# Kernel tuning notes

Hardware: AMD Instinct MI355X
Metric: run time of the kernel (lower is better)

Reference implementation:

```python
import jax, jax.numpy as jnp
import numpy as np
from jax import lax

B, C = 16, 80
LEVELS = [(100, 128), (50, 64), (25, 32), (13, 16), (7, 8)]
STRIDES = [8, 16, 32, 64, 128]
SCORE_THR = 0.05
IOU_THR = 0.6
MAX_DET = 1000


def make_coords(h, w, stride):
    # FCOS: center of each cell in original-image coordinates, order (x, y)
    ys = jnp.arange(h, dtype=jnp.float32) * stride + stride // 2
    xs = jnp.arange(w, dtype=jnp.float32) * stride + stride // 2
    yy, xx = jnp.meshgrid(ys, xs, indexing='ij')
    return jnp.stack([xx.reshape(-1), yy.reshape(-1)], axis=-1)  # [h*w, 2]


def flatten_levels(feats):
    # list of [B, c, h, w] -> [B, sum(h*w), c]
    return jnp.concatenate(
        [f.transpose(0, 2, 3, 1).reshape(f.shape[0], -1, f.shape[1]) for f in feats], axis=1)


def pairwise_iou(boxes):
    # boxes [N,4]; +1 area convention, matching the torch box_nms
    x1, y1, x2, y2 = boxes[:, 0], boxes[:, 1], boxes[:, 2], boxes[:, 3]
    areas = (x2 - x1 + 1.0) * (y2 - y1 + 1.0)
    xmin = jnp.maximum(x1[:, None], x1[None, :])
    ymin = jnp.maximum(y1[:, None], y1[None, :])
    xmax = jnp.minimum(x2[:, None], x2[None, :])
    ymax = jnp.minimum(y2[:, None], y2[None, :])
    inter = jnp.clip(xmax - xmin, 0.0) * jnp.clip(ymax - ymin, 0.0)
    return inter / (areas[:, None] + areas[None, :] - inter)


def nms_keep_mask(boxes, valid, thr):
    # boxes are sorted by descending score (top_k sorted=True) -> greedy order = index order
    n = boxes.shape[0]
    iou = pairwise_iou(boxes)
    idx = jnp.arange(n)

    def body(i, sup):
        kept = jnp.logical_not(sup[i])
        return sup | (kept & (iou[i] > thr) & (idx > i))

    sup = lax.fori_loop(0, n, body, jnp.logical_not(valid))
    return valid & jnp.logical_not(sup)


def detect_forward(cls_feats, ctr_feats, reg_feats):
    cls_logits = flatten_levels(cls_feats)   # [B, P, C]
    ctr_logits = flatten_levels(ctr_feats)   # [B, P, 1]
    reg_preds = flatten_levels(reg_feats)    # [B, P, 4] (l, t, r, b)
    coords = jnp.concatenate(
        [make_coords(h, w, s) for (h, w), s in zip(LEVELS, STRIDES)], axis=0)  # [P, 2]

    cls_preds = jax.nn.sigmoid(cls_logits)
    ctr_preds = jax.nn.sigmoid(ctr_logits)[..., 0]
    cls_scores = jnp.max(cls_preds, axis=-1) * ctr_preds        # add_centerness=True
    cls_classes = jnp.argmax(cls_preds, axis=-1) + 1            # [B, P] int

    boxes = jnp.concatenate(
        [coords[None] - reg_preds[..., :2], coords[None] + reg_preds[..., 2:]], axis=-1)

    max_num = min(MAX_DET, cls_scores.shape[-1])
    scores_topk, topk_ind = lax.top_k(cls_scores, max_num)      # sorted descending
    classes_topk = jnp.take_along_axis(cls_classes, topk_ind, axis=1)
    boxes_topk = jnp.take_along_axis(boxes, topk_ind[..., None], axis=1)

    valid = scores_topk >= SCORE_THR
    # batched_nms class-offset trick
    max_coord = jnp.max(boxes_topk, axis=(1, 2), keepdims=True)
    offs = classes_topk.astype(boxes_topk.dtype)[..., None] * (max_coord + 1.0)
    boxes_for_nms = boxes_topk + offs

    keep = jax.vmap(lambda b, v: nms_keep_mask(b, v, IOU_THR))(boxes_for_nms, valid)
    keep_f = keep.astype(scores_topk.dtype)
    # fixed-shape masked outputs (torch version returns ragged per-batch lists)
    return scores_topk * keep_f, classes_topk * keep, boxes_topk * keep_f[..., None]


def setup_inputs() -> dict:
    key = jax.random.key(0)
    ks = jax.random.split(key, 3 * len(LEVELS))
    inp = {}
    for i, (h, w) in enumerate(LEVELS):
        inp[f'cls{i}'] = jax.random.normal(ks[3 * i], (B, C, h, w), jnp.float32)
        inp[f'ctr{i}'] = jax.random.normal(ks[3 * i + 1], (B, 1, h, w), jnp.float32)
        # positive ltrb offsets of plausible magnitude
        inp[f'reg{i}'] = jax.random.uniform(ks[3 * i + 2], (B, 4, h, w), jnp.float32) * 64.0 + 1.0
    return inp


def reference(cls0, cls1, cls2, cls3, cls4, ctr0, ctr1, ctr2, ctr3, ctr4,
              reg0, reg1, reg2, reg3, reg4):
    return detect_forward([cls0, cls1, cls2, cls3, cls4],
                          [ctr0, ctr1, ctr2, ctr3, ctr4],
                          [reg0, reg1, reg2, reg3, reg4])
```

## Files before the change

### kernel.cpp

```cpp
#include <hip/hip_runtime.h>
#include <stdint.h>

#define NANCH 17064
#define BATCH 16
#define NCLS 80
#define KDET 1000
#define SCORE_THR 0.05f
#define IOU_THR 0.6f

typedef unsigned long long u64;
typedef unsigned int u32;

__device__ __forceinline__ float sigf(float x) { return 1.0f / (1.0f + expf(-x)); }

__device__ __forceinline__ void decode_anchor(int n, int& l, int& h, int& w) {
  if (n < 12800)      { l = 0; h = n >> 7;               w = n & 127; }
  else if (n < 16000) { l = 1; int r = n - 12800; h = r >> 6; w = r & 63; }
  else if (n < 16800) { l = 2; int r = n - 16000; h = r >> 5; w = r & 31; }
  else if (n < 17008) { l = 3; int r = n - 16800; h = r >> 4; w = r & 15; }
  else                { l = 4; int r = n - 17008; h = r >> 3; w = r & 7; }
}

__device__ __forceinline__ u32 fenc(float f) {
  u32 u = __float_as_uint(f);
  return (u & 0x80000000u) ? ~u : (u | 0x80000000u);
}
__device__ __forceinline__ float fdec(u32 e) {
  u32 u = (e & 0x80000000u) ? (e ^ 0x80000000u) : ~e;
  return __uint_as_float(u);
}

__global__ __launch_bounds__(256, 4) void k_score(
    const float* __restrict__ cls0, const float* __restrict__ ctr0,
    const float* __restrict__ cls1, const float* __restrict__ ctr1,
    const float* __restrict__ cls2, const float* __restrict__ ctr2,
    const float* __restrict__ cls3, const float* __restrict__ ctr3,
    const float* __restrict__ cls4, const float* __restrict__ ctr4,
    u32* __restrict__ sb, u32* __restrict__ cl8)
{
  __shared__ float sm[4][64][5];
  __shared__ u32 sa[4][64];

  const int x = threadIdx.x;
  const int y = threadIdx.y;
  const int b = blockIdx.y;
  int q = blockIdx.x * 64 + x;
  const bool act = (q < NANCH / 4);
  int qc = act ? q : (NANCH / 4 - 1);
  int n = qc * 4;

  const float* cp; const float* tp; int hw, off;
  if (n < 12800)      { cp = cls0; tp = ctr0; hw = 12800; off = n; }
  else if (n < 16000) { cp = cls1; tp = ctr1; hw = 3200;  off = n - 12800; }
  else if (n < 16800) { cp = cls2; tp = ctr2; hw = 800;   off = n - 16000; }
  else if (n < 17008) { cp = cls3; tp = ctr3; hw = 208;   off = n - 16800; }
  else                { cp = cls4; tp = ctr4; hw = 56;    off = n - 17008; }
  const float4* base = (const float4*)(cp + (size_t)b * NCLS * hw + off);
  const int s4 = hw >> 2;
  const int cb = y * 20;

  float4 v[20];
#pragma unroll
  for (int cc = 0; cc < 20; ++cc) v[cc] = base[(size_t)(cb + cc) * s4];

  float m0 = -1.0f, m1 = -1.0f, m2 = -1.0f, m3 = -1.0f;
  int a0 = 0, a1 = 0, a2 = 0, a3 = 0;
#pragma unroll
  for (int cc = 0; cc < 20; ++cc) {
    int c = cb + cc;
    float s;
    s = sigf(v[cc].x); if (s > m0) { m0 = s; a0 = c; }
    s = sigf(v[cc].y); if (s > m1) { m1 = s; a1 = c; }
    s = sigf(v[cc].z); if (s > m2) { m2 = s; a2 = c; }
    s = sigf(v[cc].w); if (s > m3) { m3 = s; a3 = c; }
  }
  sm[y][x][0] = m0; sm[y][x][1] = m1; sm[y][x][2] = m2; sm[y][x][3] = m3;
  sa[y][x] = (u32)a0 | ((u32)a1 << 8) | ((u32)a2 << 16) | ((u32)a3 << 24);
  __syncthreads();

  if (y == 0 && act) {
#pragma unroll
    for (int k = 1; k < 4; ++k) {
      u32 pk = sa[k][x];
      float t;
      t = sm[k][x][0]; if (t > m0) { m0 = t; a0 = (int)(pk & 0xffu); }
      t = sm[k][x][1]; if (t > m1) { m1 = t; a1 = (int)((pk >> 8) & 0xffu); }
      t = sm[k][x][2]; if (t > m2) { m2 = t; a2 = (int)((pk >> 16) & 0xffu); }
      t = sm[k][x][3]; if (t > m3) { m3 = t; a3 = (int)((pk >> 24) & 0xffu); }
    }
    float4 ctv = *(const float4*)(tp + (size_t)b * hw + off);
    uint4 sv;
    sv.x = __float_as_uint(m0 * sigf(ctv.x));
    sv.y = __float_as_uint(m1 * sigf(ctv.y));
    sv.z = __float_as_uint(m2 * sigf(ctv.z));
    sv.w = __float_as_uint(m3 * sigf(ctv.w));
    *(uint4*)(sb + b * NANCH + n) = sv;
    cl8[(b * NANCH + n) >> 2] = (u32)a0 | ((u32)a1 << 8) | ((u32)a2 << 16) | ((u32)a3 << 24);
  }
}

__global__ __launch_bounds__(1024) void k_topk(
    const u32* __restrict__ sb,
    u64* __restrict__ candG, int* __restrict__ cntG, u32* __restrict__ maxcG)
{
  __shared__ u32 subhist[8192];
  __shared__ u32 wtot[16];
  __shared__ int s_T1, s_above, s_T2, s_cnt;

  const int tid = threadIdx.x;
  const int b = blockIdx.x;
  const int lane = tid & 63, wv = tid >> 6;
  const int cpy = tid & 7;
  const u32* sbb = sb + b * NANCH;

  u32 sc[17];
#pragma unroll
  for (int k = 0; k < 17; ++k) {
    int n = tid + (k << 10);
    sc[k] = (n < NANCH) ? sbb[n] : 0u;
  }

#pragma unroll
  for (int k = 0; k < 8; ++k) subhist[tid + (k << 10)] = 0;
  __syncthreads();
#pragma unroll
  for (int k = 0; k < 17; ++k) {
    int n = tid + (k << 10);
    if (n < NANCH) atomicAdd(&subhist[((sc[k] >> 22) << 3) + cpy], 1u);
  }
  __syncthreads();
  u32 h = 0;
#pragma unroll
  for (int c = 0; c < 8; ++c) h += subhist[(tid << 3) + c];
  __syncthreads();
#pragma unroll
  for (int k = 0; k < 8; ++k) subhist[tid + (k << 10)] = 0;
  u32 s = h;
  for (int d = 1; d < 64; d <<= 1) { u32 y = (u32)__shfl_down((int)s, d); if (lane + d < 64) s += y; }
  if (lane == 0) wtot[wv] = s;
  __syncthreads();
  {
    u32 add = 0;
    for (int w2 = wv + 1; w2 < 16; ++w2) add += wtot[w2];
    s += add;
  }
  if (s >= (u32)KDET && s - h < (u32)KDET) { s_T1 = tid; s_above = (int)(s - h); }
  __syncthreads();
  const int T1 = s_T1; const int above = s_above;

#pragma unroll
  for (int k = 0; k < 17; ++k) {
    int n = tid + (k << 10);
    u32 bits = sc[k];
    if (n < NANCH && (int)(bits >> 22) == T1)
      atomicAdd(&subhist[(((bits >> 12) & 1023u) << 3) + cpy], 1u);
  }
  __syncthreads();
  h = 0;
#pragma unroll
  for (int c = 0; c < 8; ++c) h += subhist[(tid << 3) + c];
  s = h;
  for (int d = 1; d < 64; d <<= 1) { u32 y = (u32)__shfl_down((int)s, d); if (lane + d < 64) s += y; }
  if (lane == 0) wtot[wv] = s;
  __syncthreads();
  {
    u32 add = 0;
    for (int w2 = wv + 1; w2 < 16; ++w2) add += wtot[w2];
    s += add;
  }
  if (above + (int)s >= KDET && above + (int)(s - h) < KDET) s_T2 = tid;
  if (tid == 0) s_cnt = 0;
  __syncthreads();
  const int T2 = s_T2;

#pragma unroll
  for (int k = 0; k < 17; ++k) {
    int n = tid + (k << 10);
    u32 bits = sc[k];
    int c1 = (int)(bits >> 22);
    bool cand = (n < NANCH) &&
                ((c1 > T1) || (c1 == T1 && (int)((bits >> 12) & 1023u) >= T2));
    if (cand) {
      int pos = atomicAdd(&s_cnt, 1);
      if (pos < 2048) candG[b * 2048 + pos] = ((u64)bits << 32) | (u64)(u32)(~(u32)n);
    }
  }
  __syncthreads();
  if (tid == 0) {
    int C = s_cnt; if (C > 2048) C = 2048;
    cntG[b] = C;
    maxcG[b] = 0u;
  }
}

__global__ __launch_bounds__(256) void k_rank(
    const float* __restrict__ reg0, const float* __restrict__ reg1,
    const float* __restrict__ reg2, const float* __restrict__ reg3,
    const float* __restrict__ reg4,
    const unsigned char* __restrict__ cl8,
    const u64* __restrict__ candG, const int* __restrict__ cntG,
    float* __restrict__ scoreG, int* __restrict__ clsG, float4* __restrict__ boxG,
    u32* __restrict__ maxcG)
{
  __shared__ ulonglong2 keys2[1024];
  const int tid = threadIdx.x;
  const int c = blockIdx.x;
  const int b = blockIdx.y;
  const int lane = tid & 63;
  const int C = cntG[b];
  const u64* cand = candG + b * 2048;

  for (int i = tid; i < 1024; i += 256) {
    int i0 = 2 * i, i1 = 2 * i + 1;
    ulonglong2 v;
    v.x = (i0 < C) ? cand[i0] : 0ull;
    v.y = (i1 < C) ? cand[i1] : 0ull;
    keys2[i] = v;
  }
  __syncthreads();

  const int idx = c * 256 + tid;
  const bool active = (idx < C);
  u64 key = active ? cand[idx] : 0ull;

  int cnt = 0;
  const int Cp2 = ((C + 7) >> 3) << 2;
  for (int s = 0; s < Cp2; s += 4) {
    ulonglong2 a0 = keys2[s], a1 = keys2[s + 1], a2 = keys2[s + 2], a3 = keys2[s + 3];
    cnt += (a0.x > key) + (a0.y > key) + (a1.x > key) + (a1.y > key)
         + (a2.x > key) + (a2.y > key) + (a3.x > key) + (a3.y > key);
  }

  u32 enc = 0u;
  if (active && cnt < KDET) {
    u32 bits = (u32)(key >> 32);
    int n = (int)(~(u32)(key & 0xFFFFFFFFull));
    float score = __uint_as_float(bits);
    int clsv = (int)cl8[b * NANCH + n] + 1;
    int l, hh, ww; decode_anchor(n, l, hh, ww);
    const float* rp; int W, ST, HF, hw;
    switch (l) {
      case 0: rp = reg0; W = 128; ST = 8;   HF = 4;  hw = 12800; break;
      case 1: rp = reg1; W = 64;  ST = 16;  HF = 8;  hw = 3200;  break;
      case 2: rp = reg2; W = 32;  ST = 32;  HF = 16; hw = 800;   break;
      case 3: rp = reg3; W = 16;  ST = 64;  HF = 32; hw = 208;   break;
      default: rp = reg4; W = 8;  ST = 128; HF = 64; hw = 56;    break;
    }
    float cx = (float)(ww * ST + HF);
    float cy = (float)(hh * ST + HF);
    const float* rb = rp + (size_t)b * 4 * hw + hh * W + ww;
    float r0 = rb[0], r1 = rb[hw], r2 = rb[2 * hw], r3 = rb[3 * hw];
    float4 bx = make_float4(cx - r0, cy - r1, cx + r2, cy + r3);
    int o = b * KDET + cnt;
    scoreG[o] = score; clsG[o] = clsv; boxG[o] = bx;
    enc = fenc(fmaxf(fmaxf(bx.x, bx.y), fmaxf(bx.z, bx.w)));
  }
  for (int d = 32; d > 0; d >>= 1) {
    u32 o = (u32)__shfl_xor((int)enc, d);
    enc = (o > enc) ? o : enc;
  }
  if (lane == 0 && enc != 0u) atomicMax(maxcG + b, enc);
}

__global__ __launch_bounds__(256) void k_mat(
    const float4* __restrict__ boxG, const int* __restrict__ clsG,
    const u32* __restrict__ maxcG, u64* __restrict__ mat)
{
  const int tid = threadIdx.x, lane = tid & 63, wv = tid >> 6;
  const int b = blockIdx.y;
  const int tile = blockIdx.x * 4 + wv;
  if (tile >= 136) return;
  int rt = 0, rem = tile;
  while (rem >= rt + 1) { rem -= rt + 1; ++rt; }
  const int wc = rem;

  const float scale = fdec(maxcG[b]) + 1.0f;

  const int j = (wc << 6) + lane;
  float jx1 = 0, jy1 = 0, jx2 = 0, jy2 = 0, aj = 0;
  if (j < KDET) {
    float4 bj = boxG[b * KDET + j];
    float off = (float)clsG[b * KDET + j] * scale;
    jx1 = bj.x + off; jy1 = bj.y + off; jx2 = bj.z + off; jy2 = bj.w + off;
    aj = (jx2 - jx1 + 1.0f) * (jy2 - jy1 + 1.0f);
  }
  const int ri = (rt << 6) + lane;
  float ix1 = 0, iy1 = 0, ix2 = 0, iy2 = 0;
  if (ri < KDET) {
    float4 bi = boxG[b * KDET + ri];
    float off = (float)clsG[b * KDET + ri] * scale;
    ix1 = bi.x + off; iy1 = bi.y + off; ix2 = bi.z + off; iy2 = bi.w + off;
  }

  u64 myword = 0ull;
  for (int r = 0; r < 64; ++r) {
    float x1 = __shfl(ix1, r), y1 = __shfl(iy1, r);
    float x2 = __shfl(ix2, r), y2 = __shfl(iy2, r);
    float ai = (x2 - x1 + 1.0f) * (y2 - y1 + 1.0f);
    int row = (rt << 6) + r;
    float xmin = fmaxf(x1, jx1), ymin = fmaxf(y1, jy1);
    float xmax = fminf(x2, jx2), ymax = fminf(y2, jy2);
    float inter = fmaxf(xmax - xmin, 0.0f) * fmaxf(ymax - ymin, 0.0f);
    float iou = inter / ((ai + aj) - inter);
    bool p = (j < row) && (j < KDET) && (iou > IOU_THR);
    u64 mm = __ballot(p);
    if (lane == r) myword = mm;
  }
  const int rowl = (rt << 6) + lane;
  if (rowl < KDET) mat[(size_t)b * (KDET * 16) + rowl * 16 + wc] = myword;
}

__global__ __launch_bounds__(1024) void k_nms(
    const u64* __restrict__ mat, const float* __restrict__ scoreG,
    const int* __restrict__ clsG, const float4* __restrict__ boxG,
    float* __restrict__ out)
{
  __shared__ u64 keptS[16];
  __shared__ int s_chg;
  const int tid = threadIdx.x;
  const int b = blockIdx.x;
  const int wv = tid >> 6, lane = tid & 63;

  float sc = (tid < KDET) ? scoreG[b * KDET + tid] : 0.0f;
  bool valid = (tid < KDET) && (sc >= SCORE_THR);

  u64 row[16];
  const u64* mrow = mat + (size_t)b * (KDET * 16) + (size_t)tid * 16;
  const int wtop = tid >> 6;
#pragma unroll
  for (int w = 0; w < 16; ++w)
    row[w] = (tid < KDET && w <= wtop) ? mrow[w] : 0ull;

  {
    u64 mb = __ballot(valid);
    if (lane == 0) keptS[wv] = mb;
  }
  __syncthreads();

  for (int it = 0; it < KDET + 1; ++it) {
    u64 sup = 0;
#pragma unroll
    for (int w = 0; w < 16; ++w)
      if (w <= wtop) sup |= keptS[w] & row[w];
    bool nk = valid && (sup == 0ull);
    u64 nw = __ballot(nk);
    if (tid == 0) s_chg = 0;
    __syncthreads();
    if (lane == 0) {
      if (nw != keptS[wv]) s_chg = 1;
      keptS[wv] = nw;
    }
    __syncthreads();
    if (s_chg == 0) break;
  }

  if (tid < KDET) {
    bool kp = ((keptS[tid >> 6] >> (tid & 63)) & 1ull) != 0ull;
    int o1 = b * KDET + tid;
    out[o1] = kp ? sc : 0.0f;
    out[BATCH * KDET + o1] = kp ? (float)clsG[o1] : 0.0f;
    float4 bx = boxG[o1];
    float* ob = out + 2 * BATCH * KDET + (size_t)o1 * 4;
    ob[0] = kp ? bx.x : 0.0f;
    ob[1] = kp ? bx.y : 0.0f;
    ob[2] = kp ? bx.z : 0.0f;
    ob[3] = kp ? bx.w : 0.0f;
  }
}

extern "C" void kernel_launch(void* const* d_in, const int* in_sizes, int n_in,
                              void* d_out, int out_size, void* d_ws, size_t ws_size,
                              hipStream_t stream) {
  const float* cls[5]; const float* ctr[5]; const float* reg[5];
  for (int i = 0; i < 5; ++i) {
    cls[i] = (const float*)d_in[3 * i + 0];
    ctr[i] = (const float*)d_in[3 * i + 1];
    reg[i] = (const float*)d_in[3 * i + 2];
  }
  char* ws = (char*)d_ws;
  u32* sb   = (u32*)ws;
  unsigned char* cl8 = (unsigned char*)(ws + 1092096);
  u64* candG = (u64*)(ws + 1365120);
  u64* mat  = (u64*)ws;
  float*  scoreG = (float*) (ws + 2048000);
  int*    clsG   = (int*)   (ws + 2112000);
  float4* boxG   = (float4*)(ws + 2176000);
  int*    cntG   = (int*)   (ws + 2432000);
  u32*    maxcG  = (u32*)   (ws + 2432064);

  dim3 g1((NANCH / 4 + 63) / 64, BATCH);
  k_score<<<g1, dim3(64, 4), 0, stream>>>(cls[0], ctr[0], cls[1], ctr[1], cls[2], ctr[2],
                                          cls[3], ctr[3], cls[4], ctr[4], sb, (u32*)cl8);
  k_topk<<<BATCH, 1024, 0, stream>>>(sb, candG, cntG, maxcG);
  k_rank<<<dim3(8, BATCH), 256, 0, stream>>>(reg[0], reg[1], reg[2], reg[3], reg[4],
                                             cl8, candG, cntG, scoreG, clsG, boxG, maxcG);
  k_mat<<<dim3(34, BATCH), 256, 0, stream>>>(boxG, clsG, maxcG, mat);
  k_nms<<<BATCH, 1024, 0, stream>>>(mat, scoreG, clsG, boxG, (float*)d_out);
}
```

Baseline: 193.6 us.

## Fuse all detection stages into one cooperative kernel with grid syncs

Merges the five kernels (score, top-k select, rank/box decode, IoU matrix, greedy NMS) into a single cooperative launch of 128 blocks of 1024 threads, separated by grid-wide barriers. The score stage is remapped so each block handles four former 256-thread blocks over three passes, and the IoU-matrix tiles are distributed across waves with a grid-stride loop. The aim is to remove inter-kernel launch gaps and tail effects. In exchange, the bandwidth-heavy score phase runs on fewer resident blocks and each grid barrier adds cost.

```diff
diff --git a/kernel.cpp b/kernel.cpp
--- a/kernel.cpp
+++ b/kernel.cpp
@@ -1,7 +1,11 @@
 #include <hip/hip_runtime.h>
+#include <hip/hip_cooperative_groups.h>
 #include <stdint.h>
 
+namespace cg = cooperative_groups;
+
 #define NANCH 17064
+#define NQUAD 4266
 #define BATCH 16
 #define NCLS 80
 #define KDET 1000
@@ -30,370 +34,379 @@
   return __uint_as_float(u);
 }
 
-__global__ __launch_bounds__(256, 4) void k_score(
-    const float* __restrict__ cls0, const float* __restrict__ ctr0,
-    const float* __restrict__ cls1, const float* __restrict__ ctr1,
-    const float* __restrict__ cls2, const float* __restrict__ ctr2,
-    const float* __restrict__ cls3, const float* __restrict__ ctr3,
-    const float* __restrict__ cls4, const float* __restrict__ ctr4,
-    u32* __restrict__ sb, u32* __restrict__ cl8)
+struct Params {
+  const float* cls0; const float* ctr0; const float* reg0;
+  const float* cls1; const float* ctr1; const float* reg1;
+  const float* cls2; const float* ctr2; const float* reg2;
+  const float* cls3; const float* ctr3; const float* reg3;
+  const float* cls4; const float* ctr4; const float* reg4;
+  u32* sb; u32* cl8; u64* candG; int* cntG; u32* maxcG;
+  float* scoreG; int* clsG; float4* boxG; u64* mat; float* out;
+};
+
+__global__ __launch_bounds__(1024, 4) void k_mega(Params p)
 {
-  __shared__ float sm[4][64][5];
-  __shared__ u32 sa[4][64];
-
-  const int x = threadIdx.x;
-  const int y = threadIdx.y;
-  const int b = blockIdx.y;
-  int q = blockIdx.x * 64 + x;
-  const bool act = (q < NANCH / 4);
-  int qc = act ? q : (NANCH / 4 - 1);
-  int n = qc * 4;
-
-  const float* cp; const float* tp; int hw, off;
-  if (n < 12800)      { cp = cls0; tp = ctr0; hw = 12800; off = n; }
-  else if (n < 16000) { cp = cls1; tp = ctr1; hw = 3200;  off = n - 12800; }
-  else if (n < 16800) { cp = cls2; tp = ctr2; hw = 800;   off = n - 16000; }
-  else if (n < 17008) { cp = cls3; tp = ctr3; hw = 208;   off = n - 16800; }
-  else                { cp = cls4; tp = ctr4; hw = 56;    off = n - 17008; }
-  const float4* base = (const float4*)(cp + (size_t)b * NCLS * hw + off);
-  const int s4 = hw >> 2;
-  const int cb = y * 20;
-
-  float4 v[20];
-#pragma unroll
-  for (int cc = 0; cc < 20; ++cc) v[cc] = base[(size_t)(cb + cc) * s4];
-
-  float m0 = -1.0f, m1 = -1.0f, m2 = -1.0f, m3 = -1.0f;
-  int a0 = 0, a1 = 0, a2 = 0, a3 = 0;
-#pragma unroll
-  for (int cc = 0; cc < 20; ++cc) {
-    int c = cb + cc;
-    float s;
-    s = sigf(v[cc].x); if (s > m0) { m0 = s; a0 = c; }
-    s = sigf(v[cc].y); if (s > m1) { m1 = s; a1 = c; }
-    s = sigf(v[cc].z); if (s > m2) { m2 = s; a2 = c; }
-    s = sigf(v[cc].w); if (s > m3) { m3 = s; a3 = c; }
+  __shared__ __align__(16) char smem[32896];
+  __shared__ int sh_T1, sh_ab, sh_T2, sh_cnt, sh_chg;
+
+  cg::grid_group grid = cg::this_grid();
+  const int tid = threadIdx.x;
+  const int blk = blockIdx.x;
+  const int lane = tid & 63;
+  const int wv = tid >> 6;
+
+  {
+    const int g = tid >> 8;
+    const int x = tid & 63;
+    const int y = (tid >> 6) & 3;
+    float* smF = (float*)smem;
+    u32*   saP = (u32*)(smem + 20480);
+    for (int pass = 0; pass < 3; ++pass) {
+      int vb = pass * 512 + blk * 4 + g;
+      int vbc = vb < 1072 ? vb : 1071;
+      int b  = vbc / 67;
+      int bx = vbc - b * 67;
+      int q  = bx * 64 + x;
+      bool act = (vb < 1072) && (q < NQUAD);
+      int qc = q < NQUAD ? q : (NQUAD - 1);
+      int n = qc * 4;
+
+      const float* cp; const float* tp; int hw, off;
+      if (n < 12800)      { cp = p.cls0; tp = p.ctr0; hw = 12800; off = n; }
+      else if (n < 16000) { cp = p.cls1; tp = p.ctr1; hw = 3200;  off = n - 12800; }
+      else if (n < 16800) { cp = p.cls2; tp = p.ctr2; hw = 800;   off = n - 16000; }
+      else if (n < 17008) { cp = p.cls3; tp = p.ctr3; hw = 208;   off = n - 16800; }
+      else                { cp = p.cls4; tp = p.ctr4; hw = 56;    off = n - 17008; }
+      const float4* base = (const float4*)(cp + (size_t)b * NCLS * hw + off);
+      const int s4 = hw >> 2;
+      const int cb = y * 20;
+
+      float4 v[20];
+#pragma unroll
+      for (int cc = 0; cc < 20; ++cc) v[cc] = base[(size_t)(cb + cc) * s4];
+
+      float m0 = -1.0f, m1 = -1.0f, m2 = -1.0f, m3 = -1.0f;
+      int a0 = 0, a1 = 0, a2 = 0, a3 = 0;
+#pragma unroll
+      for (int cc = 0; cc < 20; ++cc) {
+        int c = cb + cc;
+        float s;
+        s = sigf(v[cc].x); if (s > m0) { m0 = s; a0 = c; }
+        s = sigf(v[cc].y); if (s > m1) { m1 = s; a1 = c; }
+        s = sigf(v[cc].z); if (s > m2) { m2 = s; a2 = c; }
+        s = sigf(v[cc].w); if (s > m3) { m3 = s; a3 = c; }
+      }
+      int si = ((g * 4 + y) * 64 + x);
+      smF[si * 5 + 0] = m0; smF[si * 5 + 1] = m1;
+      smF[si * 5 + 2] = m2; smF[si * 5 + 3] = m3;
+      saP[si] = (u32)a0 | ((u32)a1 << 8) | ((u32)a2 << 16) | ((u32)a3 << 24);
+      __syncthreads();
+
+      if (y == 0 && act) {
+#pragma unroll
+        for (int k = 1; k < 4; ++k) {
+          int sk = ((g * 4 + k) * 64 + x);
+          u32 pk = saP[sk];
+          float t;
+          t = smF[sk * 5 + 0]; if (t > m0) { m0 = t; a0 = (int)(pk & 0xffu); }
+          t = smF[sk * 5 + 1]; if (t > m1) { m1 = t; a1 = (int)((pk >> 8) & 0xffu); }
+          t = smF[sk * 5 + 2]; if (t > m2) { m2 = t; a2 = (int)((pk >> 16) & 0xffu); }
+          t = smF[sk * 5 + 3]; if (t > m3) { m3 = t; a3 = (int)((pk >> 24) & 0xffu); }
+        }
+        float4 ctv = *(const float4*)(tp + (size_t)b * hw + off);
+        uint4 sv;
+        sv.x = __float_as_uint(m0 * sigf(ctv.x));
+        sv.y = __float_as_uint(m1 * sigf(ctv.y));
+        sv.z = __float_as_uint(m2 * sigf(ctv.z));
+        sv.w = __float_as_uint(m3 * sigf(ctv.w));
+        *(uint4*)(p.sb + b * NANCH + n) = sv;
+        p.cl8[(b * NANCH + n) >> 2] = (u32)a0 | ((u32)a1 << 8) | ((u32)a2 << 16) | ((u32)a3 << 24);
+      }
+      __syncthreads();
+    }
   }
-  sm[y][x][0] = m0; sm[y][x][1] = m1; sm[y][x][2] = m2; sm[y][x][3] = m3;
-  sa[y][x] = (u32)a0 | ((u32)a1 << 8) | ((u32)a2 << 16) | ((u32)a3 << 24);
-  __syncthreads();
-
-  if (y == 0 && act) {
-#pragma unroll
-    for (int k = 1; k < 4; ++k) {
-      u32 pk = sa[k][x];
-      float t;
-      t = sm[k][x][0]; if (t > m0) { m0 = t; a0 = (int)(pk & 0xffu); }
-      t = sm[k][x][1]; if (t > m1) { m1 = t; a1 = (int)((pk >> 8) & 0xffu); }
-      t = sm[k][x][2]; if (t > m2) { m2 = t; a2 = (int)((pk >> 16) & 0xffu); }
-      t = sm[k][x][3]; if (t > m3) { m3 = t; a3 = (int)((pk >> 24) & 0xffu); }
-    }
-    float4 ctv = *(const float4*)(tp + (size_t)b * hw + off);
-    uint4 sv;
-    sv.x = __float_as_uint(m0 * sigf(ctv.x));
-    sv.y = __float_as_uint(m1 * sigf(ctv.y));
-    sv.z = __float_as_uint(m2 * sigf(ctv.z));
-    sv.w = __float_as_uint(m3 * sigf(ctv.w));
-    *(uint4*)(sb + b * NANCH + n) = sv;
-    cl8[(b * NANCH + n) >> 2] = (u32)a0 | ((u32)a1 << 8) | ((u32)a2 << 16) | ((u32)a3 << 24);
+  grid.sync();
+
+  if (blk < BATCH) {
+    const int b = blk;
+    u32* subhist = (u32*)smem;
+    u32* wtot = (u32*)(smem + 32768);
+    const int cpy = tid & 7;
+    const u32* sbb = p.sb + b * NANCH;
+
+    u32 sc[17];
+#pragma unroll
+    for (int k = 0; k < 17; ++k) {
+      int n = tid + (k << 10);
+      sc[k] = (n < NANCH) ? sbb[n] : 0u;
+    }
+
+#pragma unroll
+    for (int k = 0; k < 8; ++k) subhist[tid + (k << 10)] = 0;
+    __syncthreads();
+#pragma unroll
+    for (int k = 0; k < 17; ++k) {
+      int n = tid + (k << 10);
+      if (n < NANCH) atomicAdd(&subhist[((sc[k] >> 22) << 3) + cpy], 1u);
+    }
+    __syncthreads();
+    u32 h = 0;
+#pragma unroll
+    for (int c2 = 0; c2 < 8; ++c2) h += subhist[(tid << 3) + c2];
+    __syncthreads();
+#pragma unroll
+    for (int k = 0; k < 8; ++k) subhist[tid + (k << 10)] = 0;
+    u32 s = h;
+    for (int d = 1; d < 64; d <<= 1) { u32 y2 = (u32)__shfl_down((int)s, d); if (lane + d < 64) s += y2; }
+    if (lane == 0) wtot[wv] = s;
+    __syncthreads();
+    {
+      u32 add = 0;
+      for (int w2 = wv + 1; w2 < 16; ++w2) add += wtot[w2];
+      s += add;
+    }
+    if (s >= (u32)KDET && s - h < (u32)KDET) { sh_T1 = tid; sh_ab = (int)(s - h); }
+    __syncthreads();
+    const int T1 = sh_T1; const int above = sh_ab;
+
+#pragma unroll
+    for (int k = 0; k < 17; ++k) {
+      int n = tid + (k << 10);
+      u32 bits = sc[k];
+      if (n < NANCH && (int)(bits >> 22) == T1)
+        atomicAdd(&subhist[(((bits >> 12) & 1023u) << 3) + cpy], 1u);
+    }
+    __syncthreads();
+    h = 0;
+#pragma unroll
+    for (int c2 = 0; c2 < 8; ++c2) h += subhist[(tid << 3) + c2];
+    s = h;
+    for (int d = 1; d < 64; d <<= 1) { u32 y2 = (u32)__shfl_down((int)s, d); if (lane + d < 64) s += y2; }
+    if (lane == 0) wtot[wv] = s;
+    __syncthreads();
+    {
+      u32 add = 0;
+      for (int w2 = wv + 1; w2 < 16; ++w2) add += wtot[w2];
+      s += add;
+    }
+    if (above + (int)s >= KDET && above + (int)(s - h) < KDET) sh_T2 = tid;
+    if (tid == 0) sh_cnt = 0;
+    __syncthreads();
+    const int T2 = sh_T2;
+
+#pragma unroll
+    for (int k = 0; k < 17; ++k) {
+      int n = tid + (k << 10);
+      u32 bits = sc[k];
+      int c1 = (int)(bits >> 22);
+      bool cand = (n < NANCH) &&
+                  ((c1 > T1) || (c1 == T1 && (int)((bits >> 12) & 1023u) >= T2));
+      if (cand) {
+        int pos = atomicAdd(&sh_cnt, 1);
+        if (pos < 2048) p.candG[b * 2048 + pos] = ((u64)bits << 32) | (u64)(u32)(~(u32)n);
+      }
+    }
+    __syncthreads();
+    if (tid == 0) {
+      int C = sh_cnt; if (C > 2048) C = 2048;
+      p.cntG[b] = C;
+      p.maxcG[b] = 0u;
+    }
   }
-}
-
-__global__ __launch_bounds__(1024) void k_topk(
-    const u32* __restrict__ sb,
-    u64* __restrict__ candG, int* __restrict__ cntG, u32* __restrict__ maxcG)
-{
-  __shared__ u32 subhist[8192];
-  __shared__ u32 wtot[16];
-  __shared__ int s_T1, s_above, s_T2, s_cnt;
-
-  const int tid = threadIdx.x;
-  const int b = blockIdx.x;
-  const int lane = tid & 63, wv = tid >> 6;
-  const int cpy = tid & 7;
-  const u32* sbb = sb + b * NANCH;
-
-  u32 sc[17];
-#pragma unroll
-  for (int k = 0; k < 17; ++k) {
-    int n = tid + (k << 10);
-    sc[k] = (n < NANCH) ? sbb[n] : 0u;
+  grid.sync();
+
+  {
+    const int b = blk >> 3;
+    const int c = blk & 7;
+    ulonglong2* keys2 = (ulonglong2*)smem;
+    u32* cntS = (u32*)(smem + 16384);
+    const int C = p.cntG[b];
+    const u64* cand = p.candG + b * 2048;
+
+    {
+      int i0 = 2 * tid, i1 = 2 * tid + 1;
+      ulonglong2 vv;
+      vv.x = (i0 < C) ? cand[i0] : 0ull;
+      vv.y = (i1 < C) ? cand[i1] : 0ull;
+      keys2[tid] = vv;
+    }
+    if (tid < 256) cntS[tid] = 0;
+    __syncthreads();
+
+    const int lidx = tid & 255;
+    const int g = tid >> 8;
+    const int idx = c * 256 + lidx;
+    const bool active = (idx < C);
+    u64 key = active ? cand[idx] : 0ull;
+
+    int I = (C + 7) >> 3;
+    int Iq = (I + 3) >> 2;
+    int it0 = g * Iq;
+    int it1 = I < it0 + Iq ? I : it0 + Iq;
+    int cnt = 0;
+    for (int it = it0; it < it1; ++it) {
+      int s = it * 4;
+      ulonglong2 a0 = keys2[s], a1 = keys2[s + 1], a2 = keys2[s + 2], a3 = keys2[s + 3];
+      cnt += (a0.x > key) + (a0.y > key) + (a1.x > key) + (a1.y > key)
+           + (a2.x > key) + (a2.y > key) + (a3.x > key) + (a3.y > key);
+    }
+    atomicAdd(&cntS[lidx], (u32)cnt);
+    __syncthreads();
+
+    if (g == 0) {
+      int cf = (int)cntS[lidx];
+      u32 enc = 0u;
+      if (active && cf < KDET) {
+        u32 bits = (u32)(key >> 32);
+        int n = (int)(~(u32)(key & 0xFFFFFFFFull));
+        float score = __uint_as_float(bits);
+        int clsv = (int)((const unsigned char*)p.cl8)[b * NANCH + n] + 1;
+        int l, hh, ww; decode_anchor(n, l, hh, ww);
+        const float* rp; int W, ST, HF, hw;
+        switch (l) {
+          case 0: rp = p.reg0; W = 128; ST = 8;   HF = 4;  hw = 12800; break;
+          case 1: rp = p.reg1; W = 64;  ST = 16;  HF = 8;  hw = 3200;  break;
+          case 2: rp = p.reg2; W = 32;  ST = 32;  HF = 16; hw = 800;   break;
+          case 3: rp = p.reg3; W = 16;  ST = 64;  HF = 32; hw = 208;   break;
+          default: rp = p.reg4; W = 8;  ST = 128; HF = 64; hw = 56;    break;
+        }
+        float cx = (float)(ww * ST + HF);
+        float cy = (float)(hh * ST + HF);
+        const float* rb = rp + (size_t)b * 4 * hw + hh * W + ww;
+        float r0 = rb[0], r1 = rb[hw], r2 = rb[2 * hw], r3 = rb[3 * hw];
+        float4 bx = make_float4(cx - r0, cy - r1, cx + r2, cy + r3);
+        int o = b * KDET + cf;
+        p.scoreG[o] = score; p.clsG[o] = clsv; p.boxG[o] = bx;
+        enc = fenc(fmaxf(fmaxf(bx.x, bx.y), fmaxf(bx.z, bx.w)));
+      }
+      for (int d = 32; d > 0; d >>= 1) {
+        u32 o = (u32)__shfl_xor((int)enc, d);
+        enc = (o > enc) ? o : enc;
+      }
+      if ((tid & 63) == 0 && enc != 0u) atomicMax(p.maxcG + b, enc);
+    }
   }
-
-#pragma unroll
-  for (int k = 0; k < 8; ++k) subhist[tid + (k << 10)] = 0;
-  __syncthreads();
-#pragma unroll
-  for (int k = 0; k < 17; ++k) {
-    int n = tid + (k << 10);
-    if (n < NANCH) atomicAdd(&subhist[((sc[k] >> 22) << 3) + cpy], 1u);
+  grid.sync();
+
+  {
+    for (int t = blk * 16 + wv; t < 136 * BATCH; t += 128 * 16) {
+      int b = t / 136;
+      int tile = t - b * 136;
+      int rt = 0, rem = tile;
+      while (rem >= rt + 1) { rem -= rt + 1; ++rt; }
+      const int wc = rem;
+
+      const float scale = fdec(p.maxcG[b]) + 1.0f;
+
+      const int j = (wc << 6) + lane;
+      float jx1 = 0, jy1 = 0, jx2 = 0, jy2 = 0, aj = 0;
+      if (j < KDET) {
+        float4 bj = p.boxG[b * KDET + j];
+        float off = (float)p.clsG[b * KDET + j] * scale;
+        jx1 = bj.x + off; jy1 = bj.y + off; jx2 = bj.z + off; jy2 = bj.w + off;
+        aj = (jx2 - jx1 + 1.0f) * (jy2 - jy1 + 1.0f);
+      }
+      const int ri = (rt << 6) + lane;
+      float ix1 = 0, iy1 = 0, ix2 = 0, iy2 = 0;
+      if (ri < KDET) {
+        float4 bi = p.boxG[b * KDET + ri];
+        float off = (float)p.clsG[b * KDET + ri] * scale;
+        ix1 = bi.x + off; iy1 = bi.y + off; ix2 = bi.z + off; iy2 = bi.w + off;
+      }
+
+      u64 myword = 0ull;
+      for (int r = 0; r < 64; ++r) {
+        float x1 = __shfl(ix1, r), y1 = __shfl(iy1, r);
+        float x2 = __shfl(ix2, r), y2 = __shfl(iy2, r);
+        float ai = (x2 - x1 + 1.0f) * (y2 - y1 + 1.0f);
+        int row = (rt << 6) + r;
+        float xmin = fmaxf(x1, jx1), ymin = fmaxf(y1, jy1);
+        float xmax = fminf(x2, jx2), ymax = fminf(y2, jy2);
+        float inter = fmaxf(xmax - xmin, 0.0f) * fmaxf(ymax - ymin, 0.0f);
+        float iou = inter / ((ai + aj) - inter);
+        bool pr = (j < row) && (j < KDET) && (iou > IOU_THR);
+        u64 mm = __ballot(pr);
+        if (lane == r) myword = mm;
+      }
+      const int rowl = (rt << 6) + lane;
+      if (rowl < KDET) p.mat[(size_t)b * (KDET * 16) + rowl * 16 + wc] = myword;
+    }
   }
-  __syncthreads();
-  u32 h = 0;
-#pragma unroll
-  for (int c = 0; c < 8; ++c) h += subhist[(tid << 3) + c];
-  __syncthreads();
-#pragma unroll
-  for (int k = 0; k < 8; ++k) subhist[tid + (k << 10)] = 0;
-  u32 s = h;
-  for (int d = 1; d < 64; d <<= 1) { u32 y = (u32)__shfl_down((int)s, d); if (lane + d < 64) s += y; }
-  if (lane == 0) wtot[wv] = s;
-  __syncthreads();
-  {
-    u32 add = 0;
-    for (int w2 = wv + 1; w2 < 16; ++w2) add += wtot[w2];
-    s += add;
-  }
-  if (s >= (u32)KDET && s - h < (u32)KDET) { s_T1 = tid; s_above = (int)(s - h); }
-  __syncthreads();
-  const int T1 = s_T1; const int above = s_above;
-
-#pragma unroll
-  for (int k = 0; k < 17; ++k) {
-    int n = tid + (k << 10);
-    u32 bits = sc[k];
-    if (n < NANCH && (int)(bits >> 22) == T1)
-      atomicAdd(&subhist[(((bits >> 12) & 1023u) << 3) + cpy], 1u);
-  }
-  __syncthreads();
-  h = 0;
-#pragma unroll
-  for (int c = 0; c < 8; ++c) h += subhist[(tid << 3) + c];
-  s = h;
-  for (int d = 1; d < 64; d <<= 1) { u32 y = (u32)__shfl_down((int)s, d); if (lane + d < 64) s += y; }
-  if (lane == 0) wtot[wv] = s;
-  __syncthreads();
-  {
-    u32 add = 0;
-    for (int w2 = wv + 1; w2 < 16; ++w2) add += wtot[w2];
-    s += add;
-  }
-  if (above + (int)s >= KDET && above + (int)(s - h) < KDET) s_T2 = tid;
-  if (tid == 0) s_cnt = 0;
-  __syncthreads();
-  const int T2 = s_T2;
-
-#pragma unroll
-  for (int k = 0; k < 17; ++k) {
-    int n = tid + (k << 10);
-    u32 bits = sc[k];
-    int c1 = (int)(bits >> 22);
-    bool cand = (n < NANCH) &&
-                ((c1 > T1) || (c1 == T1 && (int)((bits >> 12) & 1023u) >= T2));
-    if (cand) {
-      int pos = atomicAdd(&s_cnt, 1);
-      if (pos < 2048) candG[b * 2048 + pos] = ((u64)bits << 32) | (u64)(u32)(~(u32)n);
-    }
-  }
-  __syncthreads();
-  if (tid == 0) {
-    int C = s_cnt; if (C > 2048) C = 2048;
-    cntG[b] = C;
-    maxcG[b] = 0u;
-  }
-}
-
-__global__ __launch_bounds__(256) void k_rank(
-    const float* __restrict__ reg0, const float* __restrict__ reg1,
-    const float* __restrict__ reg2, const float* __restrict__ reg3,
-    const float* __restrict__ reg4,
-    const unsigned char* __restrict__ cl8,
-    const u64* __restrict__ candG, const int* __restrict__ cntG,
-    float* __restrict__ scoreG, int* __restrict__ clsG, float4* __restrict__ boxG,
-    u32* __restrict__ maxcG)
-{
-  __shared__ ulonglong2 keys2[1024];
-  const int tid = threadIdx.x;
-  const int c = blockIdx.x;
-  const int b = blockIdx.y;
-  const int lane = tid & 63;
-  const int C = cntG[b];
-  const u64* cand = candG + b * 2048;
-
-  for (int i = tid; i < 1024; i += 256) {
-    int i0 = 2 * i, i1 = 2 * i + 1;
-    ulonglong2 v;
-    v.x = (i0 < C) ? cand[i0] : 0ull;
-    v.y = (i1 < C) ? cand[i1] : 0ull;
-    keys2[i] = v;
-  }
-  __syncthreads();
-
-  const int idx = c * 256 + tid;
-  const bool active = (idx < C);
-  u64 key = active ? cand[idx] : 0ull;
-
-  int cnt = 0;
-  const int Cp2 = ((C + 7) >> 3) << 2;
-  for (int s = 0; s < Cp2; s += 4) {
-    ulonglong2 a0 = keys2[s], a1 = keys2[s + 1], a2 = keys2[s + 2], a3 = keys2[s + 3];
-    cnt += (a0.x > key) + (a0.y > key) + (a1.x > key) + (a1.y > key)
-         + (a2.x > key) + (a2.y > key) + (a3.x > key) + (a3.y > key);
-  }
-
-  u32 enc = 0u;
-  if (active && cnt < KDET) {
-    u32 bits = (u32)(key >> 32);
-    int n = (int)(~(u32)(key & 0xFFFFFFFFull));
-    float score = __uint_as_float(bits);
-    int clsv = (int)cl8[b * NANCH + n] + 1;
-    int l, hh, ww; decode_anchor(n, l, hh, ww);
-    const float* rp; int W, ST, HF, hw;
-    switch (l) {
-      case 0: rp = reg0; W = 128; ST = 8;   HF = 4;  hw = 12800; break;
-      case 1: rp = reg1; W = 64;  ST = 16;  HF = 8;  hw = 3200;  break;
-      case 2: rp = reg2; W = 32;  ST = 32;  HF = 16; hw = 800;   break;
-      case 3: rp = reg3; W = 16;  ST = 64;  HF = 32; hw = 208;   break;
-      default: rp = reg4; W = 8;  ST = 128; HF = 64; hw = 56;    break;
-    }
-    float cx = (float)(ww * ST + HF);
-    float cy = (float)(hh * ST + HF);
-    const float* rb = rp + (size_t)b * 4 * hw + hh * W + ww;
-    float r0 = rb[0], r1 = rb[hw], r2 = rb[2 * hw], r3 = rb[3 * hw];
-    float4 bx = make_float4(cx - r0, cy - r1, cx + r2, cy + r3);
-    int o = b * KDET + cnt;
-    scoreG[o] = score; clsG[o] = clsv; boxG[o] = bx;
-    enc = fenc(fmaxf(fmaxf(bx.x, bx.y), fmaxf(bx.z, bx.w)));
-  }
-  for (int d = 32; d > 0; d >>= 1) {
-    u32 o = (u32)__shfl_xor((int)enc, d);
-    enc = (o > enc) ? o : enc;
-  }
-  if (lane == 0 && enc != 0u) atomicMax(maxcG + b, enc);
-}
-
-__global__ __launch_bounds__(256) void k_mat(
-    const float4* __restrict__ boxG, const int* __restrict__ clsG,
-    const u32* __restrict__ maxcG, u64* __restrict__ mat)
-{
-  const int tid = threadIdx.x, lane = tid & 63, wv = tid >> 6;
-  const int b = blockIdx.y;
-  const int tile = blockIdx.x * 4 + wv;
-  if (tile >= 136) return;
-  int rt = 0, rem = tile;
-  while (rem >= rt + 1) { rem -= rt + 1; ++rt; }
-  const int wc = rem;
-
-  const float scale = fdec(maxcG[b]) + 1.0f;
-
-  const int j = (wc << 6) + lane;
-  float jx1 = 0, jy1 = 0, jx2 = 0, jy2 = 0, aj = 0;
-  if (j < KDET) {
-    float4 bj = boxG[b * KDET + j];
-    float off = (float)clsG[b * KDET + j] * scale;
-    jx1 = bj.x + off; jy1 = bj.y + off; jx2 = bj.z + off; jy2 = bj.w + off;
-    aj = (jx2 - jx1 + 1.0f) * (jy2 - jy1 + 1.0f);
-  }
-  const int ri = (rt << 6) + lane;
-  float ix1 = 0, iy1 = 0, ix2 = 0, iy2 = 0;
-  if (ri < KDET) {
-    float4 bi = boxG[b * KDET + ri];
-    float off = (float)clsG[b * KDET + ri] * scale;
-    ix1 = bi.x + off; iy1 = bi.y + off; ix2 = bi.z + off; iy2 = bi.w + off;
-  }
-
-  u64 myword = 0ull;
-  for (int r = 0; r < 64; ++r) {
-    float x1 = __shfl(ix1, r), y1 = __shfl(iy1, r);
-    float x2 = __shfl(ix2, r), y2 = __shfl(iy2, r);
-    float ai = (x2 - x1 + 1.0f) * (y2 - y1 + 1.0f);
-    int row = (rt << 6) + r;
-    float xmin = fmaxf(x1, jx1), ymin = fmaxf(y1, jy1);
-    float xmax = fminf(x2, jx2), ymax = fminf(y2, jy2);
-    float inter = fmaxf(xmax - xmin, 0.0f) * fmaxf(ymax - ymin, 0.0f);
-    float iou = inter / ((ai + aj) - inter);
-    bool p = (j < row) && (j < KDET) && (iou > IOU_THR);
-    u64 mm = __ballot(p);
-    if (lane == r) myword = mm;
-  }
-  const int rowl = (rt << 6) + lane;
-  if (rowl < KDET) mat[(size_t)b * (KDET * 16) + rowl * 16 + wc] = myword;
-}
-
-__global__ __launch_bounds__(1024) void k_nms(
-    const u64* __restrict__ mat, const float* __restrict__ scoreG,
-    const int* __restrict__ clsG, const float4* __restrict__ boxG,
-    float* __restrict__ out)
-{
-  __shared__ u64 keptS[16];
-  __shared__ int s_chg;
-  const int tid = threadIdx.x;
-  const int b = blockIdx.x;
-  const int wv = tid >> 6, lane = tid & 63;
-
-  float sc = (tid < KDET) ? scoreG[b * KDET + tid] : 0.0f;
-  bool valid = (tid < KDET) && (sc >= SCORE_THR);
-
-  u64 row[16];
-  const u64* mrow = mat + (size_t)b * (KDET * 16) + (size_t)tid * 16;
-  const int wtop = tid >> 6;
-#pragma unroll
-  for (int w = 0; w < 16; ++w)
-    row[w] = (tid < KDET && w <= wtop) ? mrow[w] : 0ull;
-
-  {
-    u64 mb = __ballot(valid);
-    if (lane == 0) keptS[wv] = mb;
-  }
-  __syncthreads();
-
-  for (int it = 0; it < KDET + 1; ++it) {
-    u64 sup = 0;
+  grid.sync();
+
+  if (blk < BATCH) {
+    const int b = blk;
+    u64* keptS = (u64*)smem;
+
+    float sc = (tid < KDET) ? p.scoreG[b * KDET + tid] : 0.0f;
+    bool valid = (tid < KDET) && (sc >= SCORE_THR);
+
+    u64 row[16];
+    const u64* mrow = p.mat + (size_t)b * (KDET * 16) + (size_t)tid * 16;
+    const int wtop = tid >> 6;
 #pragma unroll
     for (int w = 0; w < 16; ++w)
-      if (w <= wtop) sup |= keptS[w] & row[w];
-    bool nk = valid && (sup == 0ull);
-    u64 nw = __ballot(nk);
-    if (tid == 0) s_chg = 0;
-    __syncthreads();
-    if (lane == 0) {
-      if (nw != keptS[wv]) s_chg = 1;
-      keptS[wv] = nw;
-    }
-    __syncthreads();
-    if (s_chg == 0) break;
-  }
-
-  if (tid < KDET) {
-    bool kp = ((keptS[tid >> 6] >> (tid & 63)) & 1ull) != 0ull;
-    int o1 = b * KDET + tid;
-    out[o1] = kp ? sc : 0.0f;
-    out[BATCH * KDET + o1] = kp ? (float)clsG[o1] : 0.0f;
-    float4 bx = boxG[o1];
-    float* ob = out + 2 * BATCH * KDET + (size_t)o1 * 4;
-    ob[0] = kp ? bx.x : 0.0f;
-    ob[1] = kp ? bx.y : 0.0f;
-    ob[2] = kp ? bx.z : 0.0f;
-    ob[3] = kp ? bx.w : 0.0f;
+      row[w] = (tid < KDET && w <= wtop) ? mrow[w] : 0ull;
+
+    {
+      u64 mb = __ballot(valid);
+      if (lane == 0) keptS[wv] = mb;
+    }
+    __syncthreads();
+
+    for (int it = 0; it < KDET + 1; ++it) {
+      u64 sup = 0;
+#pragma unroll
+      for (int w = 0; w < 16; ++w)
+        if (w <= wtop) sup |= keptS[w] & row[w];
+      bool nk = valid && (sup == 0ull);
+      u64 nw = __ballot(nk);
+      if (tid == 0) sh_chg = 0;
+      __syncthreads();
+      if (lane == 0) {
+        if (nw != keptS[wv]) sh_chg = 1;
+        keptS[wv] = nw;
+      }
+      __syncthreads();
+      if (sh_chg == 0) break;
+    }
+
+    if (tid < KDET) {
+      bool kp = ((keptS[tid >> 6] >> (tid & 63)) & 1ull) != 0ull;
+      int o1 = b * KDET + tid;
+      p.out[o1] = kp ? sc : 0.0f;
+      p.out[BATCH * KDET + o1] = kp ? (float)p.clsG[o1] : 0.0f;
+      float4 bx = p.boxG[o1];
+      float* ob = p.out + 2 * BATCH * KDET + (size_t)o1 * 4;
+      ob[0] = kp ? bx.x : 0.0f;
+      ob[1] = kp ? bx.y : 0.0f;
+      ob[2] = kp ? bx.z : 0.0f;
+      ob[3] = kp ? bx.w : 0.0f;
+    }
   }
 }
 
 extern "C" void kernel_launch(void* const* d_in, const int* in_sizes, int n_in,
                               void* d_out, int out_size, void* d_ws, size_t ws_size,
                               hipStream_t stream) {
-  const float* cls[5]; const float* ctr[5]; const float* reg[5];
-  for (int i = 0; i < 5; ++i) {
-    cls[i] = (const float*)d_in[3 * i + 0];
-    ctr[i] = (const float*)d_in[3 * i + 1];
-    reg[i] = (const float*)d_in[3 * i + 2];
-  }
   char* ws = (char*)d_ws;
-  u32* sb   = (u32*)ws;
-  unsigned char* cl8 = (unsigned char*)(ws + 1092096);
-  u64* candG = (u64*)(ws + 1365120);
-  u64* mat  = (u64*)ws;
-  float*  scoreG = (float*) (ws + 2048000);
-  int*    clsG   = (int*)   (ws + 2112000);
-  float4* boxG   = (float4*)(ws + 2176000);
-  int*    cntG   = (int*)   (ws + 2432000);
-  u32*    maxcG  = (u32*)   (ws + 2432064);
-
-  dim3 g1((NANCH / 4 + 63) / 64, BATCH);
-  k_score<<<g1, dim3(64, 4), 0, stream>>>(cls[0], ctr[0], cls[1], ctr[1], cls[2], ctr[2],
-                                          cls[3], ctr[3], cls[4], ctr[4], sb, (u32*)cl8);
-  k_topk<<<BATCH, 1024, 0, stream>>>(sb, candG, cntG, maxcG);
-  k_rank<<<dim3(8, BATCH), 256, 0, stream>>>(reg[0], reg[1], reg[2], reg[3], reg[4],
-                                             cl8, candG, cntG, scoreG, clsG, boxG, maxcG);
-  k_mat<<<dim3(34, BATCH), 256, 0, stream>>>(boxG, clsG, maxcG, mat);
-  k_nms<<<BATCH, 1024, 0, stream>>>(mat, scoreG, clsG, boxG, (float*)d_out);
+  Params p;
+  p.cls0 = (const float*)d_in[0];  p.ctr0 = (const float*)d_in[1];  p.reg0 = (const float*)d_in[2];
+  p.cls1 = (const float*)d_in[3];  p.ctr1 = (const float*)d_in[4];  p.reg1 = (const float*)d_in[5];
+  p.cls2 = (const float*)d_in[6];  p.ctr2 = (const float*)d_in[7];  p.reg2 = (const float*)d_in[8];
+  p.cls3 = (const float*)d_in[9];  p.ctr3 = (const float*)d_in[10]; p.reg3 = (const float*)d_in[11];
+  p.cls4 = (const float*)d_in[12]; p.ctr4 = (const float*)d_in[13]; p.reg4 = (const float*)d_in[14];
+  p.sb    = (u32*)ws;
+  p.cl8   = (u32*)(ws + 1092096);
+  p.candG = (u64*)(ws + 1365120);
+  p.mat   = (u64*)ws;
+  p.scoreG = (float*) (ws + 2048000);
+  p.clsG   = (int*)   (ws + 2112000);
+  p.boxG   = (float4*)(ws + 2176000);
+  p.cntG   = (int*)   (ws + 2432000);
+  p.maxcG  = (u32*)   (ws + 2432064);
+  p.out    = (float*)d_out;
+
+  void* args[] = { &p };
+  hipLaunchCooperativeKernel((void*)k_mega, dim3(128), dim3(1024), args, 0, stream);
 }
```

Result: slower. 330.8 us (+70.9%).
